# Kernel optimization log

Measured on AMD Instinct MI355X. Metric: run time of the kernel, lower is better.

The kernel has to match this reference:

```python
import jax, jax.numpy as jnp
import numpy as np

B, S, H = 8, 4096, 2048
TOP_K = 32


def setup_inputs() -> dict:
    key = jax.random.key(0)
    k1, k2, k3 = jax.random.split(key, 3)
    base = jax.random.normal(k1, (B, S, H), dtype=jnp.float32)
    batch_weights = jax.random.normal(k2, (B, 1, H), dtype=jnp.float32)
    intervention_positions = jax.random.randint(k3, (B, S), 0, S, dtype=jnp.int32)
    return {"base": base, "intervention_positions": intervention_positions,
            "batch_weights": batch_weights}


def reference(base, intervention_positions, batch_weights):
    # base: [B,S,H]; intervention_positions: [B,S]; batch_weights: [B,1,H]
    b, s, h = base.shape
    bidx = jnp.arange(b)[:, None]                                   # [B,1]
    # gather intervened hidden states: base[b, pos]  -> [B,S,H]
    gathered = jnp.take_along_axis(base, intervention_positions[..., None], axis=1)
    # psi(h) = ReLU(W h): rank-1 bmm with batch_weights -> [B,S]
    detect_latent = jax.nn.relu(
        jnp.einsum('bsh,bh->bs', gathered, batch_weights[:, 0, :]))
    topk_vals, topk_idx = jax.lax.top_k(detect_latent, TOP_K)       # [B,K]
    # zero out the top-k entries (scatter along last dim)
    non_topk_latents = detect_latent.at[bidx, topk_idx].set(0.0)
    # steering vector: mean(topk) * W  -> [B,1,H]
    steer = jnp.mean(topk_vals, axis=-1)[:, None, None] * batch_weights
    # scatter-add steering vector back at the intervened positions
    mixed_output = base.at[bidx, intervention_positions].add(
        jnp.broadcast_to(steer, (b, s, h)))
    return mixed_output, detect_latent, non_topk_latents
```

## Files before the change

kernel.cpp:

```cpp
#include <hip/hip_runtime.h>

#define TOPK 32

__global__ void detect_kernel(const float* __restrict__ base,
                              const int* __restrict__ pos,
                              const float* __restrict__ bw,
                              float* __restrict__ detect,
                              int* __restrict__ counts,
                              int S, int H) {
    int wid  = (blockIdx.x * blockDim.x + threadIdx.x) >> 6;
    int lane = threadIdx.x & 63;
    int b = wid / S;
    int s = wid - b * S;
    int p = pos[b * S + s];

    const float4* row = (const float4*)(base + ((size_t)b * S + p) * H);
    const float4* w4  = (const float4*)(bw + (size_t)b * H);
    int n4 = H >> 2;

    float acc = 0.f;
    for (int i = lane; i < n4; i += 64) {
        float4 v = row[i];
        float4 w = w4[i];
        acc += v.x * w.x + v.y * w.y + v.z * w.z + v.w * w.w;
    }
    for (int off = 32; off > 0; off >>= 1)
        acc += __shfl_down(acc, off, 64);

    if (lane == 0) {
        detect[b * S + s] = fmaxf(acc, 0.f);
        atomicAdd(&counts[b * S + p], 1);
    }
}

__global__ void topk_kernel(const float* __restrict__ detect,
                            float* __restrict__ nontopk,
                            float* __restrict__ meanv,
                            int S) {
    extern __shared__ float vals[];
    __shared__ float wval[4];
    __shared__ int   widx[4];

    int b = blockIdx.x;
    int t = threadIdx.x;

    for (int i = t; i < S; i += 256) vals[i] = detect[(size_t)b * S + i];
    __syncthreads();

    float sum = 0.f;
    for (int it = 0; it < TOPK; ++it) {
        float lv = -INFINITY;
        int   li = 0x7fffffff;
        for (int i = t; i < S; i += 256) {
            float v = vals[i];
            if (v > lv) { lv = v; li = i; }
        }
        for (int off = 32; off > 0; off >>= 1) {
            float ov = __shfl_down(lv, off, 64);
            int   oi = __shfl_down(li, off, 64);
            if (ov > lv || (ov == lv && oi < li)) { lv = ov; li = oi; }
        }
        int lane = t & 63, w = t >> 6;
        if (lane == 0) { wval[w] = lv; widx[w] = li; }
        __syncthreads();
        if (t == 0) {
            float bv = wval[0]; int bi = widx[0];
            for (int k = 1; k < 4; ++k)
                if (wval[k] > bv || (wval[k] == bv && widx[k] < bi)) { bv = wval[k]; bi = widx[k]; }
            sum += bv;
            vals[bi] = -INFINITY;
            if (it == TOPK - 1) meanv[b] = sum / (float)TOPK;
        }
        __syncthreads();
    }

    for (int i = t; i < S; i += 256) {
        float v = vals[i];
        nontopk[(size_t)b * S + i] = (v == -INFINITY) ? 0.f : v;
    }
}

__global__ void mix_kernel(const float* __restrict__ base,
                           const float* __restrict__ bw,
                           const int* __restrict__ counts,
                           const float* __restrict__ meanv,
                           float* __restrict__ mixed,
                           int S, int H) {
    int row = blockIdx.x;
    int b = row / S;
    float scale = (float)counts[row] * meanv[b];

    const float4* b4 = (const float4*)(base + (size_t)row * H);
    const float4* w4 = (const float4*)(bw + (size_t)b * H);
    float4*       o4 = (float4*)(mixed + (size_t)row * H);
    int n4 = H >> 2;

    for (int i = threadIdx.x; i < n4; i += blockDim.x) {
        float4 v = b4[i];
        float4 w = w4[i];
        v.x += scale * w.x;
        v.y += scale * w.y;
        v.z += scale * w.z;
        v.w += scale * w.w;
        o4[i] = v;
    }
}

extern "C" void kernel_launch(void* const* d_in, const int* in_sizes, int n_in,
                              void* d_out, int out_size, void* d_ws, size_t ws_size,
                              hipStream_t stream) {
    const float* base = (const float*)d_in[0];
    const int*   pos  = (const int*)d_in[1];
    const float* bw   = (const float*)d_in[2];

    long n0 = in_sizes[0];
    long n1 = in_sizes[1];
    long n2 = in_sizes[2];
    int H = (int)(n0 / n1);
    int B = (int)(n2 / H);
    int S = (int)(n1 / B);

    float* out_mixed   = (float*)d_out;
    float* out_detect  = out_mixed + (size_t)B * S * H;
    float* out_nontopk = out_detect + (size_t)B * S;

    int*   counts = (int*)d_ws;
    float* meanv  = (float*)((char*)d_ws + (size_t)B * S * sizeof(int));

    hipMemsetAsync(counts, 0, (size_t)B * S * sizeof(int), stream);

    int nwaves = B * S;
    detect_kernel<<<nwaves / 4, 256, 0, stream>>>(base, pos, bw, out_detect, counts, S, H);
    topk_kernel<<<B, 256, (size_t)S * sizeof(float), stream>>>(out_detect, out_nontopk, meanv, S);
    mix_kernel<<<B * S, 256, 0, stream>>>(base, bw, counts, meanv, out_mixed, S, H);
}
```

Measured before the change: 189.0 us.

## Compute dots on contiguous rows then gather scores inside fused top-k kernel

```diff
diff --git a/kernel.cpp b/kernel.cpp
--- a/kernel.cpp
+++ b/kernel.cpp
@@ -2,59 +2,75 @@
 
 #define TOPK 32
 
-__global__ void detect_kernel(const float* __restrict__ base,
-                              const int* __restrict__ pos,
-                              const float* __restrict__ bw,
-                              float* __restrict__ detect,
-                              int* __restrict__ counts,
-                              int S, int H) {
+__global__ void dot_kernel(const float* __restrict__ base,
+                           const float* __restrict__ bw,
+                           float* __restrict__ d2,
+                           int S, int H) {
     int wid  = (blockIdx.x * blockDim.x + threadIdx.x) >> 6;
     int lane = threadIdx.x & 63;
     int b = wid / S;
-    int s = wid - b * S;
-    int p = pos[b * S + s];
 
-    const float4* row = (const float4*)(base + ((size_t)b * S + p) * H);
+    const float4* row = (const float4*)(base + (size_t)wid * H);
     const float4* w4  = (const float4*)(bw + (size_t)b * H);
     int n4 = H >> 2;
 
     float acc = 0.f;
+    #pragma unroll 8
     for (int i = lane; i < n4; i += 64) {
         float4 v = row[i];
         float4 w = w4[i];
         acc += v.x * w.x + v.y * w.y + v.z * w.z + v.w * w.w;
     }
+    #pragma unroll
     for (int off = 32; off > 0; off >>= 1)
         acc += __shfl_down(acc, off, 64);
 
-    if (lane == 0) {
-        detect[b * S + s] = fmaxf(acc, 0.f);
-        atomicAdd(&counts[b * S + p], 1);
-    }
+    if (lane == 0) d2[wid] = acc;
 }
 
-__global__ void topk_kernel(const float* __restrict__ detect,
-                            float* __restrict__ nontopk,
-                            float* __restrict__ meanv,
-                            int S) {
-    extern __shared__ float vals[];
-    __shared__ float wval[4];
-    __shared__ int   widx[4];
+__global__ void topk_fused_kernel(const float* __restrict__ d2,
+                                  const int* __restrict__ pos,
+                                  float* __restrict__ detect,
+                                  float* __restrict__ nontopk,
+                                  int* __restrict__ counts,
+                                  float* __restrict__ meanv,
+                                  int S) {
+    extern __shared__ float smem[];
+    float* dvals = smem;
+    float* vals  = smem + S;
+    int*   cnt   = (int*)(smem + 2 * S);
+    __shared__ float wval[16];
+    __shared__ int   widx[16];
 
     int b = blockIdx.x;
     int t = threadIdx.x;
+    int T = blockDim.x;
+    int nw = T >> 6;
 
-    for (int i = t; i < S; i += 256) vals[i] = detect[(size_t)b * S + i];
+    for (int i = t; i < S; i += T) {
+        dvals[i] = d2[(size_t)b * S + i];
+        cnt[i] = 0;
+    }
+    __syncthreads();
+
+    for (int i = t; i < S; i += T) {
+        int p = pos[(size_t)b * S + i];
+        float v = fmaxf(dvals[p], 0.f);
+        vals[i] = v;
+        detect[(size_t)b * S + i] = v;
+        atomicAdd(&cnt[p], 1);
+    }
     __syncthreads();
 
     float sum = 0.f;
     for (int it = 0; it < TOPK; ++it) {
         float lv = -INFINITY;
         int   li = 0x7fffffff;
-        for (int i = t; i < S; i += 256) {
+        for (int i = t; i < S; i += T) {
             float v = vals[i];
             if (v > lv) { lv = v; li = i; }
         }
+        #pragma unroll
         for (int off = 32; off > 0; off >>= 1) {
             float ov = __shfl_down(lv, off, 64);
             int   oi = __shfl_down(li, off, 64);
@@ -65,7 +81,7 @@
         __syncthreads();
         if (t == 0) {
             float bv = wval[0]; int bi = widx[0];
-            for (int k = 1; k < 4; ++k)
+            for (int k = 1; k < nw; ++k)
                 if (wval[k] > bv || (wval[k] == bv && widx[k] < bi)) { bv = wval[k]; bi = widx[k]; }
             sum += bv;
             vals[bi] = -INFINITY;
@@ -74,9 +90,10 @@
         __syncthreads();
     }
 
-    for (int i = t; i < S; i += 256) {
+    for (int i = t; i < S; i += T) {
         float v = vals[i];
         nontopk[(size_t)b * S + i] = (v == -INFINITY) ? 0.f : v;
+        counts[(size_t)b * S + i] = cnt[i];
     }
 }
 
@@ -95,6 +112,7 @@
     float4*       o4 = (float4*)(mixed + (size_t)row * H);
     int n4 = H >> 2;
 
+    #pragma unroll 2
     for (int i = threadIdx.x; i < n4; i += blockDim.x) {
         float4 v = b4[i];
         float4 w = w4[i];
@@ -125,12 +143,12 @@
     float* out_nontopk = out_detect + (size_t)B * S;
 
     int*   counts = (int*)d_ws;
-    float* meanv  = (float*)((char*)d_ws + (size_t)B * S * sizeof(int));
+    float* d2     = (float*)((char*)d_ws + (size_t)B * S * sizeof(int));
+    float* meanv  = (float*)((char*)d_ws + 2 * (size_t)B * S * sizeof(int));
 
-    hipMemsetAsync(counts, 0, (size_t)B * S * sizeof(int), stream);
-
-    int nwaves = B * S;
-    detect_kernel<<<nwaves / 4, 256, 0, stream>>>(base, pos, bw, out_detect, counts, S, H);
-    topk_kernel<<<B, 256, (size_t)S * sizeof(float), stream>>>(out_detect, out_nontopk, meanv, S);
-    mix_kernel<<<B * S, 256, 0, stream>>>(base, bw, counts, meanv, out_mixed, S, H);
+    int nrows = B * S;
+    dot_kernel<<<nrows / 4, 256, 0, stream>>>(base, bw, d2, S, H);
+    topk_fused_kernel<<<B, 1024, 3 * (size_t)S * sizeof(float), stream>>>(
+        d2, pos, out_detect, out_nontopk, counts, meanv, S);
+    mix_kernel<<<nrows, 256, 0, stream>>>(base, bw, counts, meanv, out_mixed, S, H);
 }
```

Measured after the change: 223.9 us. 18.5% more time.
